# Kernel optimization log

Hardware: AMD Instinct MI355X
Metric: run time of the kernel (lower is better)

The kernel has to match this reference:

```python
import jax, jax.numpy as jnp
import numpy as np

N, E, D_IN, D_H, D_OUT, W = 100000, 1600000, 128, 128, 128, 3
HTC_W, TEMP = 0.01, 1.0  # curvature c = 1.0


def _project(x):
    n = jnp.maximum(jnp.linalg.norm(x, axis=-1, keepdims=True), 1e-12)
    return x * jnp.minimum((1.0 - 1e-5) / n, 1.0)


def _artanh(x):
    x = jnp.clip(x, -1.0 + 1e-6, 1.0 - 1e-6)
    return 0.5 * (jnp.log1p(x) - jnp.log1p(-x))


def _expmap0(v):
    n = jnp.maximum(jnp.linalg.norm(v, axis=-1, keepdims=True), 1e-12)
    return _project(jnp.tanh(n) * v / n)


def _logmap0(y):
    y = _project(y)
    n = jnp.maximum(jnp.linalg.norm(y, axis=-1, keepdims=True), 1e-12)
    return _artanh(n) * y / n


def setup_inputs() -> dict:
    key = jax.random.key(0)
    ks = jax.random.split(key, 24)
    x = jax.random.normal(ks[0], (N, D_IN), dtype=jnp.float32)
    edge_index = jax.random.randint(ks[1], (2, E), 0, N)
    t = jax.random.uniform(ks[2], (E,), dtype=jnp.float32)
    prev_hyp = _project(jax.random.normal(ks[3], (N, D_OUT), dtype=jnp.float32) * 0.05)
    lengths = jax.random.randint(ks[4], (N,), 0, W + 1)
    valid_mask = jnp.arange(W)[None, :] < lengths[:, None]  # front-filled deque
    hist_hyp = _project(jax.random.normal(ks[5], (N, W, D_OUT), dtype=jnp.float32) * 0.05)
    hist_hyp = hist_hyp * valid_mask[..., None].astype(jnp.float32)  # padded slots are zero

    def lin(k, dout, din):
        return jax.random.normal(k, (dout, din), dtype=jnp.float32) / np.sqrt(din)

    params = dict(
        w_time=jax.random.normal(ks[6], (D_IN,), dtype=jnp.float32),
        b_time=jnp.zeros((D_IN,), jnp.float32),
        W0_l=lin(ks[7], D_H, D_IN), b0_l=jnp.zeros((D_H,), jnp.float32), W0_r=lin(ks[8], D_H, D_IN),
        W1_l=lin(ks[9], D_OUT, D_H), b1_l=jnp.zeros((D_OUT,), jnp.float32), W1_r=lin(ks[10], D_OUT, D_H),
        W_ih=lin(ks[11], 3 * D_OUT, D_OUT), W_hh=lin(ks[12], 3 * D_OUT, D_OUT),
        b_ih=jnp.zeros((3 * D_OUT,), jnp.float32), b_hh=jnp.zeros((3 * D_OUT,), jnp.float32),
        Wq=lin(ks[13], D_OUT, D_OUT), Wk=lin(ks[14], D_OUT, D_OUT), Wv=lin(ks[15], D_OUT, D_OUT),
    )
    return dict(x=x, edge_index=edge_index, t=t, prev_hyp=prev_hyp,
                hist_hyp=hist_hyp, valid_mask=valid_mask, **params)


def reference(x, edge_index, t, prev_hyp, hist_hyp, valid_mask,
              w_time, b_time, W0_l, b0_l, W0_r, W1_l, b1_l, W1_r,
              W_ih, W_hh, b_ih, b_hh, Wq, Wk, Wv):
    n = x.shape[0]
    src, dst = edge_index[0], edge_index[1]
    ones_e = jnp.ones_like(t)
    # per-node mean event time over incident edges (src and dst both count)
    nt = jax.ops.segment_sum(t, src, n) + jax.ops.segment_sum(t, dst, n)
    cnt = jax.ops.segment_sum(ones_e, src, n) + jax.ops.segment_sum(ones_e, dst, n)
    node_time = nt / jnp.maximum(cnt, 1.0)
    x = x + jnp.cos(node_time[:, None] * w_time[None, :] + b_time[None, :])
    # SAGEConv (mean aggr over incoming edges): out = W_l @ mean_j x_j + b + W_r @ x_i
    deg = jnp.maximum(jax.ops.segment_sum(ones_e, dst, n), 1.0)[:, None]
    agg0 = jax.ops.segment_sum(x[src], dst, n) / deg
    h = jax.nn.relu(agg0 @ W0_l.T + b0_l + x @ W0_r.T)
    agg1 = jax.ops.segment_sum(h[src], dst, n) / deg
    h_now = agg1 @ W1_l.T + b1_l + h @ W1_r.T  # tangent-space current embedding

    prev_tan = _logmap0(prev_hyp)
    # ragged history attention (padded + masked)
    hist_tan = _logmap0(hist_hyp)                       # [N, W, D]
    q = h_now @ Wq.T                                    # [N, D]
    k = hist_tan @ Wk.T                                 # [N, W, D]
    v = hist_tan @ Wv.T
    score = jnp.einsum('nwd,nd->nw', k, q) / (np.sqrt(D_OUT) * max(TEMP, 1e-6))
    has_hist = valid_mask.any(axis=-1, keepdims=True)
    score = jnp.where(valid_mask, score, -jnp.inf)
    score = jnp.where(has_hist, score, 0.0)
    alpha = jax.nn.softmax(score, axis=-1)
    alpha = jnp.where(has_hist, alpha, 0.0)
    ctx = jnp.einsum('nw,nwd->nd', alpha, v)

    # GRUCell(input=h_now, hidden=prev_tan + ctx)
    hidden = prev_tan + ctx
    gi = h_now @ W_ih.T + b_ih
    gh = hidden @ W_hh.T + b_hh
    i_r, i_z, i_n = jnp.split(gi, 3, axis=-1)
    h_r, h_z, h_n = jnp.split(gh, 3, axis=-1)
    r = jax.nn.sigmoid(i_r + h_r)
    z = jax.nn.sigmoid(i_z + h_z)
    nn_ = jnp.tanh(i_n + r * h_n)
    h_tan = (1.0 - z) * nn_ + z * hidden
    h_hyp = _expmap0(h_tan)

    # hyperbolic temporal consistency aux loss (c = 1)
    x_sq = jnp.sum(h_hyp * h_hyp, axis=-1)
    y_sq = jnp.sum(prev_hyp * prev_hyp, axis=-1)
    diff_sq = jnp.sum((h_hyp - prev_hyp) ** 2, axis=-1)
    denom = jnp.maximum((1.0 - x_sq) * (1.0 - y_sq), 1e-8)
    zarg = jnp.maximum(1.0 + 2.0 * diff_sq / denom, 1.0 + 1e-6)
    dist = jnp.arccosh(zarg)
    valid_prev = (jnp.sum(jnp.abs(prev_hyp), axis=-1) > 0).astype(dist.dtype)
    aux = HTC_W * jnp.sum(dist * valid_prev) / jnp.maximum(jnp.sum(valid_prev), 1.0)
    aux = jnp.where(jnp.any(valid_prev > 0), aux, 0.0)
    return h_hyp, aux
```

## Files before the change

kernel.cpp:

```cpp
#include <hip/hip_runtime.h>
#include <math.h>


typedef _Float16 f16x8 __attribute__((ext_vector_type(8)));
typedef _Float16 f16x4 __attribute__((ext_vector_type(4)));
typedef _Float16 f16x2 __attribute__((ext_vector_type(2)));
typedef float f32x4 __attribute__((ext_vector_type(4)));

__device__ __forceinline__ float wsum(float v) {
#pragma unroll
  for (int off = 1; off < 64; off <<= 1) v += __shfl_xor(v, off, 64);
  return v;
}

__device__ __forceinline__ void fsplit(float x, _Float16& h, _Float16& l) {
  h = (_Float16)x;
  l = (_Float16)(x - (float)h);
}

__device__ __forceinline__ float logmap_scale(float nrm2) {
  float n0 = fmaxf(sqrtf(nrm2), 1e-12f);
  float sp = fminf((1.0f - 1e-5f) / n0, 1.0f);
  float np = fmaxf(n0 * sp, 1e-12f);
  float a  = fminf(np, 1.0f - 1e-6f);
  float at = 0.5f * (log1pf(a) - log1pf(-a));
  return sp * at / np;
}

__global__ void k_edge(const int* __restrict__ ei, const float* __restrict__ t,
                       unsigned long long* __restrict__ packed, int E) {
  int e = blockIdx.x * 256 + threadIdx.x;
  if (e >= E) return;
  int s = ei[e], d = ei[E + e];
  unsigned long long tf =
      (unsigned long long)__float2uint_rn(t[e] * 16777216.0f);
  unsigned long long encs = tf | (1ULL << 40);
  atomicAdd(&packed[s], encs);
  atomicAdd(&packed[d], encs | (1ULL << 52));
}

__global__ void k_scan1(const unsigned long long* __restrict__ packed,
                        int* __restrict__ rowptr, int* __restrict__ bsum, int N) {
  __shared__ int s[256];
  int t = threadIdx.x;
  int base = blockIdx.x * 1024 + t * 4;
  int v[4]; int loc = 0;
#pragma unroll
  for (int j = 0; j < 4; ++j) {
    int i = base + j;
    v[j] = (i < N) ? (int)(packed[i] >> 52) : 0;
    loc += v[j];
  }
  s[t] = loc; __syncthreads();
  for (int off = 1; off < 256; off <<= 1) {
    int x = (t >= off) ? s[t - off] : 0; __syncthreads();
    s[t] += x; __syncthreads();
  }
  int run = s[t] - loc;
#pragma unroll
  for (int j = 0; j < 4; ++j) { int i = base + j; if (i < N) rowptr[i] = run; run += v[j]; }
  if (t == 255) bsum[blockIdx.x] = s[255];
}

__global__ void k_scan2(const int* __restrict__ bsum, int* __restrict__ boff, int nb) {
  __shared__ int s[128];
  int t = threadIdx.x;
  int v = (t < nb) ? bsum[t] : 0;
  s[t] = v; __syncthreads();
  for (int off = 1; off < 128; off <<= 1) {
    int x = (t >= off) ? s[t - off] : 0; __syncthreads();
    s[t] += x; __syncthreads();
  }
  boff[t] = s[t] - v;
}

__global__ void k_scan3(int* __restrict__ rowptr, const int* __restrict__ boff, int N, int E) {
  int i = blockIdx.x * 256 + threadIdx.x;
  if (i < N) rowptr[i] += boff[i >> 10];
  if (i == 0) rowptr[N] = E;
}

__global__ void k_scatter(const int* __restrict__ ei, const int* __restrict__ rowptr,
                          int* __restrict__ cursor, int* __restrict__ eidx, int E) {
  int e = blockIdx.x * 256 + threadIdx.x;
  if (e >= E) return;
  int s = ei[e], d = ei[E + e];
  int p = rowptr[d] + atomicAdd(&cursor[d], 1);
  eidx[p] = s;
}

__global__ void k_time(const float* __restrict__ x,
                       const unsigned long long* __restrict__ packed,
                       const float* __restrict__ wt,
                       const float* __restrict__ bt,
                       _Float16* __restrict__ outH, _Float16* __restrict__ outL, int N) {
  int id = blockIdx.x * 256 + threadIdx.x;
  if (id >= N * 32) return;
  int n = id >> 5, q = id & 31;
  unsigned long long p = packed[n];
  float tsum = (float)(p & 0xFFFFFFFFFFULL) * 5.9604644775390625e-8f;
  int c = (int)((p >> 40) & 0xFFF);
  float tm = tsum / fmaxf((float)c, 1.0f);
  float4 xv = ((const float4*)x)[id];
  float4 wv = ((const float4*)wt)[q];
  float4 bv = ((const float4*)bt)[q];
  float o[4];
  o[0] = xv.x + cosf(tm * wv.x + bv.x);
  o[1] = xv.y + cosf(tm * wv.y + bv.y);
  o[2] = xv.z + cosf(tm * wv.z + bv.z);
  o[3] = xv.w + cosf(tm * wv.w + bv.w);
  f16x4 vh, vl;
#pragma unroll
  for (int j = 0; j < 4; ++j) { _Float16 h, l; fsplit(o[j], h, l); vh[j] = h; vl[j] = l; }
  *(f16x4*)&outH[(size_t)id * 4] = vh;
  *(f16x4*)&outL[(size_t)id * 4] = vl;
}

__global__ void k_agg(const _Float16* __restrict__ XH, const _Float16* __restrict__ XL,
                      const int* __restrict__ rowptr,
                      const int* __restrict__ eidx, _Float16* __restrict__ outH,
                      _Float16* __restrict__ outL, int N) {
  int wid = threadIdx.x >> 6, lane = threadIdx.x & 63;
  int n = blockIdx.x * 4 + wid;
  if (n >= N) return;
  int s0 = rowptr[n], s1 = rowptr[n + 1];
  float ax = 0.f, ay = 0.f;
  for (int e = s0; e < s1; ++e) {
    int s = eidx[e];
    f16x2 vh = *(const f16x2*)&XH[(size_t)s * 128 + lane * 2];
    f16x2 vl = *(const f16x2*)&XL[(size_t)s * 128 + lane * 2];
    ax += (float)vh[0] + (float)vl[0];
    ay += (float)vh[1] + (float)vl[1];
  }
  float sc = 1.0f / fmaxf((float)(s1 - s0), 1.0f);
  _Float16 hx, lx, hy, ly;
  fsplit(ax * sc, hx, lx); fsplit(ay * sc, hy, ly);
  f16x2 vh = {hx, hy}, vl = {lx, ly};
  *(f16x2*)&outH[(size_t)n * 128 + lane * 2] = vh;
  *(f16x2*)&outL[(size_t)n * 128 + lane * 2] = vl;
}

__global__ void k_prep(const float* __restrict__ W0l, const float* __restrict__ W0r,
                       const float* __restrict__ W1l, const float* __restrict__ W1r,
                       const float* __restrict__ Wv,  const float* __restrict__ Wih,
                       const float* __restrict__ Whh, const float* __restrict__ bih,
                       const float* __restrict__ bhh,
                       _Float16* __restrict__ W0H, _Float16* __restrict__ W0L,
                       _Float16* __restrict__ W1H, _Float16* __restrict__ W1L,
                       _Float16* __restrict__ WvH, _Float16* __restrict__ WvL,
                       _Float16* __restrict__ WzH, _Float16* __restrict__ WzL,
                       float* __restrict__ bz) {
  int id = blockIdx.x * 256 + threadIdx.x;
  if (id < 32768) {
    int c = id >> 8, k = id & 255;
    float v0 = (k < 128) ? W0l[c * 128 + k] : W0r[c * 128 + (k - 128)];
    float v1 = (k < 128) ? W1l[c * 128 + k] : W1r[c * 128 + (k - 128)];
    fsplit(v0, W0H[id], W0L[id]);
    fsplit(v1, W1H[id], W1L[id]);
  }
  if (id < 16384) {
    fsplit(Wv[id], WvH[id], WvL[id]);
  }
  if (id < 131072) {
    int c = id >> 8, k = id & 255;
    float v;
    if (c < 256)      v = (k < 128) ? Wih[c * 128 + k] : Whh[c * 128 + (k - 128)];
    else if (c < 384) v = (k < 128) ? Wih[c * 128 + k] : 0.f;
    else              v = (k < 128) ? 0.f : Whh[(c - 128) * 128 + (k - 128)];
    fsplit(v, WzH[id], WzL[id]);
  }
  if (id < 512) {
    float v;
    if (id < 256)      v = bih[id] + bhh[id];
    else if (id < 384) v = bih[id];
    else               v = bhh[id - 128];
    bz[id] = v;
  }
}

__global__ void k_ct(const float* __restrict__ Wk, const float* __restrict__ Wq,
                     _Float16* __restrict__ CtH, _Float16* __restrict__ CtL) {
  int id = blockIdx.x * 256 + threadIdx.x;
  if (id >= 16384) return;
  int c = id >> 7, k = id & 127;
  float s = 0.f;
  for (int j = 0; j < 128; ++j) s += Wk[j * 128 + c] * Wq[j * 128 + k];
  fsplit(s, CtH[id], CtL[id]);
}

__global__ __launch_bounds__(256)
void k_mm(const _Float16* __restrict__ A1H, const _Float16* __restrict__ A1L,
          const _Float16* __restrict__ A2H, const _Float16* __restrict__ A2L,
          const _Float16* __restrict__ WH,  const _Float16* __restrict__ WL,
          const float* __restrict__ bias,   const float* __restrict__ addb,
          float* __restrict__ outF, _Float16* __restrict__ outH,
          _Float16* __restrict__ outL,
          int Nrows, int Ktot, int Ctot, int relu) {
  __shared__ _Float16 sA[2][128][64];
  __shared__ _Float16 sW[2][128][64];
  const int tid = threadIdx.x;
  const int lane = tid & 63;
  const int wv = tid >> 6;
  const int wr = wv >> 1, wc = wv & 1;
  const int laneR = lane & 15, laneG = lane >> 4;
  const int n0 = blockIdx.x * 128;
  const int c0 = blockIdx.y * 128;

  f32x4 acc[4][4];
#pragma unroll
  for (int mi = 0; mi < 4; ++mi)
#pragma unroll
    for (int ni = 0; ni < 4; ++ni)
#pragma unroll
      for (int j = 0; j < 4; ++j) acc[mi][ni][j] = 0.f;

  const int nslab = Ktot >> 6;
  for (int s = 0; s < nslab; ++s) {
    int kglob = s << 6;
    const _Float16* aH = (kglob < 128) ? A1H : A2H;
    const _Float16* aL = (kglob < 128) ? A1L : A2L;
    int kc = kglob & 127;
    __syncthreads();
#pragma unroll
    for (int it = 0; it < 4; ++it) {
      int idx = tid + (it << 8);
      int r = idx >> 3, chunk = idx & 7;
      int cs = (chunk ^ (r & 7)) << 3;
      int kq = chunk << 3;
      int n = n0 + r;
      f16x8 vh, vl;
      if (n < Nrows) {
        vh = *(const f16x8*)&aH[(size_t)n * 128 + kc + kq];
        vl = *(const f16x8*)&aL[(size_t)n * 128 + kc + kq];
      } else {
#pragma unroll
        for (int j = 0; j < 8; ++j) { vh[j] = (_Float16)0; vl[j] = (_Float16)0; }
      }
      *(f16x8*)&sA[0][r][cs] = vh;
      *(f16x8*)&sA[1][r][cs] = vl;
      int c = c0 + r;
      f16x8 wh = *(const f16x8*)&WH[(size_t)c * Ktot + kglob + kq];
      f16x8 wl = *(const f16x8*)&WL[(size_t)c * Ktot + kglob + kq];
      *(f16x8*)&sW[0][r][cs] = wh;
      *(f16x8*)&sW[1][r][cs] = wl;
    }
    __syncthreads();
#pragma unroll
    for (int kk = 0; kk < 2; ++kk) {
      f16x8 ah[4], al[4], bh[4], bl[4];
      int kch = (kk << 2) + laneG;
#pragma unroll
      for (int m = 0; m < 4; ++m) {
        int row = wr * 64 + m * 16 + laneR;
        int ko = (kch ^ (row & 7)) << 3;
        ah[m] = *(const f16x8*)&sA[0][row][ko];
        al[m] = *(const f16x8*)&sA[1][row][ko];
      }
#pragma unroll
      for (int n = 0; n < 4; ++n) {
        int row = wc * 64 + n * 16 + laneR;
        int ko = (kch ^ (row & 7)) << 3;
        bh[n] = *(const f16x8*)&sW[0][row][ko];
        bl[n] = *(const f16x8*)&sW[1][row][ko];
      }
#pragma unroll
      for (int m = 0; m < 4; ++m)
#pragma unroll
        for (int n = 0; n < 4; ++n) {
          acc[m][n] = __builtin_amdgcn_mfma_f32_16x16x32_f16(ah[m], bh[n], acc[m][n], 0, 0, 0);
          acc[m][n] = __builtin_amdgcn_mfma_f32_16x16x32_f16(al[m], bh[n], acc[m][n], 0, 0, 0);
          acc[m][n] = __builtin_amdgcn_mfma_f32_16x16x32_f16(ah[m], bl[n], acc[m][n], 0, 0, 0);
        }
    }
  }
#pragma unroll
  for (int m = 0; m < 4; ++m) {
#pragma unroll
    for (int n = 0; n < 4; ++n) {
      int rbase = n0 + wr * 64 + m * 16 + laneG * 4;
      int c = c0 + wc * 64 + n * 16 + laneR;
      float bval = bias ? bias[c] : 0.f;
#pragma unroll
      for (int j = 0; j < 4; ++j) {
        int r = rbase + j;
        if (r >= Nrows) continue;
        float v = acc[m][n][j] + bval;
        if (addb) v += addb[(size_t)r * Ctot + c];
        if (relu) v = fmaxf(v, 0.f);
        if (outF) outF[(size_t)r * Ctot + c] = v;
        if (outH) {
          _Float16 h, l; fsplit(v, h, l);
          outH[(size_t)r * Ctot + c] = h;
          outL[(size_t)r * Ctot + c] = l;
        }
      }
    }
  }
}

__global__ __launch_bounds__(256, 2)
void k_gru(const _Float16* __restrict__ P0H, const _Float16* __restrict__ P0L,
           const _Float16* __restrict__ P2H, const _Float16* __restrict__ P2L,
           const _Float16* __restrict__ WzH, const _Float16* __restrict__ WzL,
           const float* __restrict__ bz, const float* __restrict__ prev,
           float* __restrict__ out, float* __restrict__ pd,
           float* __restrict__ pv, int N) {
  __shared__ _Float16 sA[2][64][64];
  __shared__ _Float16 sW[2][128][64];
  __shared__ float rn1[64][2];
  __shared__ float rn3[64][2][3];
  __shared__ float distrow[64], validrow[64];
  const int tid = threadIdx.x;
  const int lane = tid & 63;
  const int wv = tid >> 6;
  const int wr = wv >> 1, wc = wv & 1;
  const int laneR = lane & 15, laneG = lane >> 4;
  const int n0 = blockIdx.x * 64;

  f32x4 acc[4][2][4];
#pragma unroll
  for (int q = 0; q < 4; ++q)
#pragma unroll
    for (int m = 0; m < 2; ++m)
#pragma unroll
      for (int n = 0; n < 4; ++n)
#pragma unroll
        for (int j = 0; j < 4; ++j) acc[q][m][n][j] = 0.f;

#define STAGE_W(Q)                                                          \
  {                                                                         \
    _Pragma("unroll")                                                       \
    for (int it = 0; it < 4; ++it) {                                        \
      int idx = tid + (it << 8);                                            \
      int r = idx >> 3, chunk = idx & 7;                                    \
      int cs = (chunk ^ (r & 7)) << 3;                                      \
      int kq = chunk << 3;                                                  \
      size_t wrow = (size_t)((Q)*128 + r);                                  \
      *(f16x8*)&sW[0][r][cs] = *(const f16x8*)&WzH[wrow * 256 + kglob + kq];\
      *(f16x8*)&sW[1][r][cs] = *(const f16x8*)&WzL[wrow * 256 + kglob + kq];\
    }                                                                       \
  }

#define COMPUTE_Q(Q)                                                        \
  {                                                                         \
    _Pragma("unroll")                                                       \
    for (int kk = 0; kk < 2; ++kk) {                                        \
      int kch = (kk << 2) + laneG;                                          \
      f16x8 ah[2], al[2], bh[4], bl[4];                                     \
      _Pragma("unroll")                                                     \
      for (int m = 0; m < 2; ++m) {                                         \
        int row = wr * 32 + m * 16 + laneR;                                 \
        int ko = (kch ^ (row & 7)) << 3;                                    \
        ah[m] = *(const f16x8*)&sA[0][row][ko];                             \
        al[m] = *(const f16x8*)&sA[1][row][ko];                             \
      }                                                                     \
      _Pragma("unroll")                                                     \
      for (int n = 0; n < 4; ++n) {                                         \
        int row = wc * 64 + n * 16 + laneR;                                 \
        int ko = (kch ^ (row & 7)) << 3;                                    \
        bh[n] = *(const f16x8*)&sW[0][row][ko];                             \
        bl[n] = *(const f16x8*)&sW[1][row][ko];                             \
      }                                                                     \
      _Pragma("unroll")                                                     \
      for (int m = 0; m < 2; ++m)                                           \
        _Pragma("unroll")                                                   \
        for (int n = 0; n < 4; ++n) {                                       \
          acc[Q][m][n] = __builtin_amdgcn_mfma_f32_16x16x32_f16(ah[m], bh[n], acc[Q][m][n], 0, 0, 0); \
          acc[Q][m][n] = __builtin_amdgcn_mfma_f32_16x16x32_f16(al[m], bh[n], acc[Q][m][n], 0, 0, 0); \
          acc[Q][m][n] = __builtin_amdgcn_mfma_f32_16x16x32_f16(ah[m], bl[n], acc[Q][m][n], 0, 0, 0); \
        }                                                                   \
    }                                                                       \
  }

#pragma unroll
  for (int s = 0; s < 4; ++s) {
    int kglob = s << 6;
    const _Float16* aH = (s < 2) ? P0H : P2H;
    const _Float16* aL = (s < 2) ? P0L : P2L;
    int kc = kglob & 127;
    __syncthreads();
#pragma unroll
    for (int it = 0; it < 2; ++it) {
      int idx = tid + (it << 8);
      int r = idx >> 3, chunk = idx & 7;
      int cs = (chunk ^ (r & 7)) << 3;
      int kq = chunk << 3;
      int n = n0 + r;
      f16x8 vh, vl;
      if (n < N) {
        vh = *(const f16x8*)&aH[(size_t)n * 128 + kc + kq];
        vl = *(const f16x8*)&aL[(size_t)n * 128 + kc + kq];
      } else {
#pragma unroll
        for (int j = 0; j < 8; ++j) { vh[j] = (_Float16)0; vl[j] = (_Float16)0; }
      }
      *(f16x8*)&sA[0][r][cs] = vh;
      *(f16x8*)&sA[1][r][cs] = vl;
    }
    STAGE_W(0);
    __syncthreads();
    COMPUTE_Q(0);
    __syncthreads();
    STAGE_W(1);
    __syncthreads();
    COMPUTE_Q(1);
    __syncthreads();
    if (s < 2) {
      STAGE_W(2);
      __syncthreads();
      COMPUTE_Q(2);
    } else {
      STAGE_W(3);
      __syncthreads();
      COMPUTE_Q(3);
    }
  }
#undef STAGE_W
#undef COMPUTE_Q

  float bz0[4], bz1[4], bz2[4], bz3[4];
#pragma unroll
  for (int n = 0; n < 4; ++n) {
    int d = wc * 64 + n * 16 + laneR;
    bz0[n] = bz[d]; bz1[n] = bz[128 + d]; bz2[n] = bz[256 + d]; bz3[n] = bz[384 + d];
  }
  float tv[2][4][4];
#pragma unroll
  for (int m = 0; m < 2; ++m)
#pragma unroll
    for (int n = 0; n < 4; ++n)
#pragma unroll
      for (int j = 0; j < 4; ++j) {
        int row = n0 + wr * 32 + m * 16 + laneG * 4 + j;
        int d = wc * 64 + n * 16 + laneR;
        float hid = 0.f;
        if (row < N) {
          size_t o = (size_t)row * 128 + d;
          hid = (float)P2H[o] + (float)P2L[o];
        }
        float gr = acc[0][m][n][j] + bz0[n];
        float gz = acc[1][m][n][j] + bz1[n];
        float gi = acc[2][m][n][j] + bz2[n];
        float gh = acc[3][m][n][j] + bz3[n];
        float rr = 1.f / (1.f + expf(-gr));
        float zz = 1.f / (1.f + expf(-gz));
        float nn = tanhf(gi + rr * gh);
        tv[m][n][j] = (1.f - zz) * nn + zz * hid;
      }
#pragma unroll
  for (int m = 0; m < 2; ++m)
#pragma unroll
    for (int j = 0; j < 4; ++j) {
      float p = 0.f;
#pragma unroll
      for (int n = 0; n < 4; ++n) p += tv[m][n][j] * tv[m][n][j];
#pragma unroll
      for (int off = 1; off < 16; off <<= 1) p += __shfl_xor(p, off, 64);
      if (laneR == 0) rn1[wr * 32 + m * 16 + laneG * 4 + j][wc] = p;
    }
  __syncthreads();
  float hv[2][4][4];
#pragma unroll
  for (int m = 0; m < 2; ++m)
#pragma unroll
    for (int j = 0; j < 4; ++j) {
      int rl = wr * 32 + m * 16 + laneG * 4 + j;
      int row = n0 + rl;
      float nv2 = rn1[rl][0] + rn1[rl][1];
      float nv = fmaxf(sqrtf(nv2), 1e-12f);
      float tn = tanhf(nv);
      float s1 = tn / nv;
      float nw = fmaxf(tn, 1e-12f);
      float sp = fminf((1.f - 1e-5f) / nw, 1.f);
      float scl = s1 * sp;
#pragma unroll
      for (int n = 0; n < 4; ++n) {
        float h = tv[m][n][j] * scl;
        hv[m][n][j] = h;
        int d = wc * 64 + n * 16 + laneR;
        if (row < N) out[(size_t)row * 128 + d] = h;
      }
    }
#pragma unroll
  for (int m = 0; m < 2; ++m)
#pragma unroll
    for (int j = 0; j < 4; ++j) {
      int rl = wr * 32 + m * 16 + laneG * 4 + j;
      int row = n0 + rl;
      float ys = 0.f, ds = 0.f, pa = 0.f;
#pragma unroll
      for (int n = 0; n < 4; ++n) {
        int d = wc * 64 + n * 16 + laneR;
        float p = (row < N) ? prev[(size_t)row * 128 + d] : 0.f;
        float h = hv[m][n][j];
        ys += p * p; ds += (h - p) * (h - p); pa += fabsf(p);
      }
#pragma unroll
      for (int off = 1; off < 16; off <<= 1) {
        ys += __shfl_xor(ys, off, 64);
        ds += __shfl_xor(ds, off, 64);
        pa += __shfl_xor(pa, off, 64);
      }
      if (laneR == 0) { rn3[rl][wc][0] = ys; rn3[rl][wc][1] = ds; rn3[rl][wc][2] = pa; }
    }
  __syncthreads();
  if (wc == 0 && laneR == 0) {
#pragma unroll
    for (int m = 0; m < 2; ++m)
#pragma unroll
      for (int j = 0; j < 4; ++j) {
        int rl = wr * 32 + m * 16 + laneG * 4 + j;
        int row = n0 + rl;
        float nv2 = rn1[rl][0] + rn1[rl][1];
        float nv = fmaxf(sqrtf(nv2), 1e-12f);
        float tn = tanhf(nv);
        float s1 = tn / nv;
        float nw = fmaxf(tn, 1e-12f);
        float sp = fminf((1.f - 1e-5f) / nw, 1.f);
        float scl = s1 * sp;
        float x_sq = scl * scl * nv2;
        float y_sq = rn3[rl][0][0] + rn3[rl][1][0];
        float d_sq = rn3[rl][0][1] + rn3[rl][1][1];
        float pab  = rn3[rl][0][2] + rn3[rl][1][2];
        float denom = fmaxf((1.f - x_sq) * (1.f - y_sq), 1e-8f);
        float zarg = fmaxf(1.f + 2.f * d_sq / denom, 1.f + 1e-6f);
        float dist = acoshf(zarg);
        float valid = (pab > 0.f && row < N) ? 1.f : 0.f;
        distrow[rl] = dist * valid;
        validrow[rl] = valid;
      }
  }
  __syncthreads();
  if (tid < 64) {
    float dv = distrow[tid], vvv = validrow[tid];
    dv = wsum(dv); vvv = wsum(vvv);
    if (tid == 0) { pd[blockIdx.x] = dv; pv[blockIdx.x] = vvv; }
  }
}

__global__ void k_logmap(const float* __restrict__ Y, float* __restrict__ out, int N) {
  int wid = threadIdx.x >> 6, lane = threadIdx.x & 63;
  int n = blockIdx.x * 4 + wid;
  if (n >= N) return;
  float2 y = ((const float2*)Y)[(size_t)n * 64 + lane];
  float nrm2 = wsum(y.x * y.x + y.y * y.y);
  float s = logmap_scale(nrm2);
  ((float2*)out)[(size_t)n * 64 + lane] = make_float2(y.x * s, y.y * s);
}

__global__ void k_attn(const float* __restrict__ U, const float* __restrict__ hist,
                       _Float16* __restrict__ outH, _Float16* __restrict__ outL, int N) {
  int wid = threadIdx.x >> 6, lane = threadIdx.x & 63;
  int n = blockIdx.x * 4 + wid;
  if (n >= N) return;
  float2 u = ((const float2*)U)[(size_t)n * 64 + lane];
  float htx[3], hty[3], sc[3];
  bool val[3];
#pragma unroll
  for (int w = 0; w < 3; ++w) {
    float2 h = ((const float2*)hist)[((size_t)n * 3 + w) * 64 + lane];
    float nrm2 = wsum(h.x * h.x + h.y * h.y);
    val[w] = nrm2 > 0.f;
    float s = logmap_scale(nrm2);
    htx[w] = h.x * s; hty[w] = h.y * s;
    float d = wsum(htx[w] * u.x + hty[w] * u.y);
    sc[w] = d * 0.0883883476483184f;
  }
  float cx = 0.f, cy = 0.f;
  if (val[0] || val[1] || val[2]) {
    float m = -INFINITY;
#pragma unroll
    for (int w = 0; w < 3; ++w) if (val[w]) m = fmaxf(m, sc[w]);
    float a[3]; float ssum = 0.f;
#pragma unroll
    for (int w = 0; w < 3; ++w) { a[w] = val[w] ? expf(sc[w] - m) : 0.f; ssum += a[w]; }
    float inv = 1.f / ssum;
#pragma unroll
    for (int w = 0; w < 3; ++w) { cx += htx[w] * (a[w] * inv); cy += hty[w] * (a[w] * inv); }
  }
  _Float16 hx, lx, hy, ly;
  fsplit(cx, hx, lx); fsplit(cy, hy, ly);
  f16x2 vh = {hx, hy}, vl = {lx, ly};
  *(f16x2*)&outH[(size_t)n * 128 + lane * 2] = vh;
  *(f16x2*)&outL[(size_t)n * 128 + lane * 2] = vl;
}

__global__ void k_reduce(const float* __restrict__ pd, const float* __restrict__ pv,
                         float* __restrict__ aux_out, int nparts) {
  __shared__ float sd[256], sv[256];
  float a = 0.f, b = 0.f;
  for (int i = threadIdx.x; i < nparts; i += 256) { a += pd[i]; b += pv[i]; }
  sd[threadIdx.x] = a; sv[threadIdx.x] = b; __syncthreads();
  for (int off = 128; off > 0; off >>= 1) {
    if (threadIdx.x < off) { sd[threadIdx.x] += sd[threadIdx.x + off]; sv[threadIdx.x] += sv[threadIdx.x + off]; }
    __syncthreads();
  }
  if (threadIdx.x == 0) {
    float aux = (sv[0] > 0.f) ? 0.01f * sd[0] / fmaxf(sv[0], 1.f) : 0.f;
    aux_out[0] = aux;
  }
}

extern "C" void kernel_launch(void* const* d_in, const int* in_sizes, int n_in,
                              void* d_out, int out_size, void* d_ws, size_t ws_size,
                              hipStream_t stream) {
  const float* x      = (const float*)d_in[0];
  const int*   ei     = (const int*)  d_in[1];
  const float* t      = (const float*)d_in[2];
  const float* prev   = (const float*)d_in[3];
  const float* hist   = (const float*)d_in[4];
  const float* w_time = (const float*)d_in[6];
  const float* b_time = (const float*)d_in[7];
  const float* W0l    = (const float*)d_in[8];
  const float* b0l    = (const float*)d_in[9];
  const float* W0r    = (const float*)d_in[10];
  const float* W1l    = (const float*)d_in[11];
  const float* b1l    = (const float*)d_in[12];
  const float* W1r    = (const float*)d_in[13];
  const float* Wih    = (const float*)d_in[14];
  const float* Whh    = (const float*)d_in[15];
  const float* bih    = (const float*)d_in[16];
  const float* bhh    = (const float*)d_in[17];
  const float* Wq     = (const float*)d_in[18];
  const float* Wk     = (const float*)d_in[19];
  const float* Wv     = (const float*)d_in[20];

  const int N = in_sizes[0] / 128;
  const int E = in_sizes[1] / 2;
  const int NB4 = (N + 3) / 4;
  const int NB1 = (N + 1023) / 1024;
  const int NBG = (N + 63) / 64;

  char* wbase = (char*)d_ws;
  size_t off = 0;
  auto alloc = [&](size_t bytes) -> void* {
    off = (off + 255) & ~(size_t)255;
    void* p = wbase + off; off += bytes; return p;
  };
  unsigned long long* packed = (unsigned long long*)alloc((size_t)N * 8);
  int*   cursor = (int*)  alloc((size_t)N * 4);
  size_t zero_bytes = off;
  int*   rowptr = (int*)  alloc((size_t)(N + 1) * 4);
  int*   bsum   = (int*)  alloc(512);
  int*   boff   = (int*)  alloc(512);
  int*   eidx   = (int*)  alloc((size_t)E * 4);
  _Float16* W0H = (_Float16*)alloc(32768 * 2);
  _Float16* W0L = (_Float16*)alloc(32768 * 2);
  _Float16* W1H = (_Float16*)alloc(32768 * 2);
  _Float16* W1L = (_Float16*)alloc(32768 * 2);
  _Float16* CtH = (_Float16*)alloc(16384 * 2);
  _Float16* CtL = (_Float16*)alloc(16384 * 2);
  _Float16* WvH = (_Float16*)alloc(16384 * 2);
  _Float16* WvL = (_Float16*)alloc(16384 * 2);
  _Float16* WzH = (_Float16*)alloc(131072 * 2);
  _Float16* WzL = (_Float16*)alloc(131072 * 2);
  float* bz     = (float*)alloc(512 * 4);
  float* F0 = (float*)alloc((size_t)N * 128 * 4);
  float* F1 = (float*)alloc((size_t)N * 128 * 4);
  _Float16* P0H = (_Float16*)alloc((size_t)N * 128 * 2);
  _Float16* P0L = (_Float16*)alloc((size_t)N * 128 * 2);
  _Float16* P1H = (_Float16*)alloc((size_t)N * 128 * 2);
  _Float16* P1L = (_Float16*)alloc((size_t)N * 128 * 2);
  _Float16* P2H = (_Float16*)alloc((size_t)N * 128 * 2);
  _Float16* P2L = (_Float16*)alloc((size_t)N * 128 * 2);
  float* pd = (float*)alloc((size_t)NBG * 4);
  float* pv = (float*)alloc((size_t)NBG * 4);
  (void)ws_size; (void)n_in; (void)out_size;

  float* out_h   = (float*)d_out;
  float* out_aux = out_h + (size_t)N * 128;

  hipMemsetAsync(d_ws, 0, zero_bytes, stream);

  k_prep<<<512, 256, 0, stream>>>(W0l, W0r, W1l, W1r, Wv, Wih, Whh, bih, bhh,
                                  W0H, W0L, W1H, W1L, WvH, WvL, WzH, WzL, bz);
  k_ct<<<64, 256, 0, stream>>>(Wk, Wq, CtH, CtL);

  int ebl = (E + 255) / 256;
  k_edge<<<ebl, 256, 0, stream>>>(ei, t, packed, E);
  k_scan1<<<NB1, 256, 0, stream>>>(packed, rowptr, bsum, N);
  k_scan2<<<1, 128, 0, stream>>>(bsum, boff, NB1);
  k_scan3<<<(N + 255) / 256, 256, 0, stream>>>(rowptr, boff, N, E);
  k_scatter<<<ebl, 256, 0, stream>>>(ei, rowptr, cursor, eidx, E);

  k_time<<<(N * 32 + 255) / 256, 256, 0, stream>>>(x, packed, w_time, b_time,
                                                   P0H, P0L, N);
  k_agg<<<NB4, 256, 0, stream>>>(P0H, P0L, rowptr, eidx, P1H, P1L, N);
  dim3 gb((N + 127) / 128, 1);
  k_mm<<<gb, 256, 0, stream>>>(P1H, P1L, P0H, P0L, W0H, W0L, b0l, nullptr,
                               nullptr, P2H, P2L, N, 256, 128, 1);
  k_agg<<<NB4, 256, 0, stream>>>(P2H, P2L, rowptr, eidx, P1H, P1L, N);
  k_mm<<<gb, 256, 0, stream>>>(P1H, P1L, P2H, P2L, W1H, W1L, b1l, nullptr,
                               nullptr, P0H, P0L, N, 256, 128, 0);
  k_mm<<<gb, 256, 0, stream>>>(P0H, P0L, nullptr, nullptr, CtH, CtL, nullptr, nullptr,
                               F0, nullptr, nullptr, N, 128, 128, 0);
  k_attn<<<NB4, 256, 0, stream>>>(F0, hist, P1H, P1L, N);
  k_logmap<<<NB4, 256, 0, stream>>>(prev, F1, N);
  k_mm<<<gb, 256, 0, stream>>>(P1H, P1L, nullptr, nullptr, WvH, WvL, nullptr, F1,
                               nullptr, P2H, P2L, N, 128, 128, 0);
  k_gru<<<NBG, 256, 0, stream>>>(P0H, P0L, P2H, P2L, WzH, WzL, bz, prev,
                                 out_h, pd, pv, N);
  k_reduce<<<1, 256, 0, stream>>>(pd, pv, out_aux, NBG);
}
```

Measured before the change: 1.224 ms.

## Fuse query-key matmul with attention and fold logmap scale into Wv epilogue

Result: no change. 1.215 ms (-0.7%).

```diff
diff --git a/kernel.cpp b/kernel.cpp
--- a/kernel.cpp
+++ b/kernel.cpp
@@ -124,11 +124,31 @@
   int n = blockIdx.x * 4 + wid;
   if (n >= N) return;
   int s0 = rowptr[n], s1 = rowptr[n + 1];
-  float ax = 0.f, ay = 0.f;
-  for (int e = s0; e < s1; ++e) {
+  size_t lo2 = (size_t)lane * 2;
+  float ax0 = 0.f, ay0 = 0.f, ax1 = 0.f, ay1 = 0.f;
+  float ax2 = 0.f, ay2 = 0.f, ax3 = 0.f, ay3 = 0.f;
+  int e = s0;
+  for (; e + 4 <= s1; e += 4) {
+    int i0 = eidx[e], i1 = eidx[e + 1], i2 = eidx[e + 2], i3 = eidx[e + 3];
+    f16x2 h0 = *(const f16x2*)&XH[(size_t)i0 * 128 + lo2];
+    f16x2 l0 = *(const f16x2*)&XL[(size_t)i0 * 128 + lo2];
+    f16x2 h1 = *(const f16x2*)&XH[(size_t)i1 * 128 + lo2];
+    f16x2 l1 = *(const f16x2*)&XL[(size_t)i1 * 128 + lo2];
+    f16x2 h2 = *(const f16x2*)&XH[(size_t)i2 * 128 + lo2];
+    f16x2 l2 = *(const f16x2*)&XL[(size_t)i2 * 128 + lo2];
+    f16x2 h3 = *(const f16x2*)&XH[(size_t)i3 * 128 + lo2];
+    f16x2 l3 = *(const f16x2*)&XL[(size_t)i3 * 128 + lo2];
+    ax0 += (float)h0[0] + (float)l0[0]; ay0 += (float)h0[1] + (float)l0[1];
+    ax1 += (float)h1[0] + (float)l1[0]; ay1 += (float)h1[1] + (float)l1[1];
+    ax2 += (float)h2[0] + (float)l2[0]; ay2 += (float)h2[1] + (float)l2[1];
+    ax3 += (float)h3[0] + (float)l3[0]; ay3 += (float)h3[1] + (float)l3[1];
+  }
+  float ax = (ax0 + ax1) + (ax2 + ax3);
+  float ay = (ay0 + ay1) + (ay2 + ay3);
+  for (; e < s1; ++e) {
     int s = eidx[e];
-    f16x2 vh = *(const f16x2*)&XH[(size_t)s * 128 + lane * 2];
-    f16x2 vl = *(const f16x2*)&XL[(size_t)s * 128 + lane * 2];
+    f16x2 vh = *(const f16x2*)&XH[(size_t)s * 128 + lo2];
+    f16x2 vl = *(const f16x2*)&XL[(size_t)s * 128 + lo2];
     ax += (float)vh[0] + (float)vl[0];
     ay += (float)vh[1] + (float)vl[1];
   }
@@ -136,8 +156,8 @@
   _Float16 hx, lx, hy, ly;
   fsplit(ax * sc, hx, lx); fsplit(ay * sc, hy, ly);
   f16x2 vh = {hx, hy}, vl = {lx, ly};
-  *(f16x2*)&outH[(size_t)n * 128 + lane * 2] = vh;
-  *(f16x2*)&outL[(size_t)n * 128 + lane * 2] = vl;
+  *(f16x2*)&outH[(size_t)n * 128 + lo2] = vh;
+  *(f16x2*)&outL[(size_t)n * 128 + lo2] = vl;
 }
 
 __global__ void k_prep(const float* __restrict__ W0l, const float* __restrict__ W0r,
@@ -188,11 +208,21 @@
   fsplit(s, CtH[id], CtL[id]);
 }
 
+__global__ void k_lognorm(const float* __restrict__ Y, float* __restrict__ scale, int N) {
+  int wid = threadIdx.x >> 6, lane = threadIdx.x & 63;
+  int n = blockIdx.x * 4 + wid;
+  if (n >= N) return;
+  float2 y = ((const float2*)Y)[(size_t)n * 64 + lane];
+  float nrm2 = wsum(y.x * y.x + y.y * y.y);
+  if (lane == 0) scale[n] = logmap_scale(nrm2);
+}
+
 __global__ __launch_bounds__(256)
 void k_mm(const _Float16* __restrict__ A1H, const _Float16* __restrict__ A1L,
           const _Float16* __restrict__ A2H, const _Float16* __restrict__ A2L,
           const _Float16* __restrict__ WH,  const _Float16* __restrict__ WL,
           const float* __restrict__ bias,   const float* __restrict__ addb,
+          const float* __restrict__ scalev,
           float* __restrict__ outF, _Float16* __restrict__ outH,
           _Float16* __restrict__ outL,
           int Nrows, int Ktot, int Ctot, int relu) {
@@ -285,7 +315,10 @@
         int r = rbase + j;
         if (r >= Nrows) continue;
         float v = acc[m][n][j] + bval;
-        if (addb) v += addb[(size_t)r * Ctot + c];
+        if (addb) {
+          float ab = addb[(size_t)r * Ctot + c];
+          v += scalev ? ab * scalev[r] : ab;
+        }
         if (relu) v = fmaxf(v, 0.f);
         if (outF) outF[(size_t)r * Ctot + c] = v;
         if (outH) {
@@ -295,6 +328,133 @@
         }
       }
     }
+  }
+}
+
+__global__ __launch_bounds__(256, 2)
+void k_uattn(const _Float16* __restrict__ AH, const _Float16* __restrict__ AL,
+             const _Float16* __restrict__ WH, const _Float16* __restrict__ WL,
+             const float* __restrict__ hist,
+             _Float16* __restrict__ outH, _Float16* __restrict__ outL, int N) {
+  __shared__ __align__(16) char smem[65536];
+  _Float16 (*sA)[128][64] = (_Float16(*)[128][64])smem;
+  _Float16 (*sW)[128][64] = (_Float16(*)[128][64])(smem + 32768);
+  float (*uS)[128] = (float(*)[128])smem;
+  const int tid = threadIdx.x;
+  const int lane = tid & 63;
+  const int wv = tid >> 6;
+  const int wr = wv >> 1, wc = wv & 1;
+  const int laneR = lane & 15, laneG = lane >> 4;
+  const int n0 = blockIdx.x * 128;
+
+  f32x4 acc[4][4];
+#pragma unroll
+  for (int mi = 0; mi < 4; ++mi)
+#pragma unroll
+    for (int ni = 0; ni < 4; ++ni)
+#pragma unroll
+      for (int j = 0; j < 4; ++j) acc[mi][ni][j] = 0.f;
+
+  for (int s = 0; s < 2; ++s) {
+    int kglob = s << 6;
+    __syncthreads();
+#pragma unroll
+    for (int it = 0; it < 4; ++it) {
+      int idx = tid + (it << 8);
+      int r = idx >> 3, chunk = idx & 7;
+      int cs = (chunk ^ (r & 7)) << 3;
+      int kq = chunk << 3;
+      int n = n0 + r;
+      f16x8 vh, vl;
+      if (n < N) {
+        vh = *(const f16x8*)&AH[(size_t)n * 128 + kglob + kq];
+        vl = *(const f16x8*)&AL[(size_t)n * 128 + kglob + kq];
+      } else {
+#pragma unroll
+        for (int j = 0; j < 8; ++j) { vh[j] = (_Float16)0; vl[j] = (_Float16)0; }
+      }
+      *(f16x8*)&sA[0][r][cs] = vh;
+      *(f16x8*)&sA[1][r][cs] = vl;
+      f16x8 wh = *(const f16x8*)&WH[(size_t)r * 128 + kglob + kq];
+      f16x8 wl = *(const f16x8*)&WL[(size_t)r * 128 + kglob + kq];
+      *(f16x8*)&sW[0][r][cs] = wh;
+      *(f16x8*)&sW[1][r][cs] = wl;
+    }
+    __syncthreads();
+#pragma unroll
+    for (int kk = 0; kk < 2; ++kk) {
+      f16x8 ah[4], al[4], bh[4], bl[4];
+      int kch = (kk << 2) + laneG;
+#pragma unroll
+      for (int m = 0; m < 4; ++m) {
+        int row = wr * 64 + m * 16 + laneR;
+        int ko = (kch ^ (row & 7)) << 3;
+        ah[m] = *(const f16x8*)&sA[0][row][ko];
+        al[m] = *(const f16x8*)&sA[1][row][ko];
+      }
+#pragma unroll
+      for (int n = 0; n < 4; ++n) {
+        int row = wc * 64 + n * 16 + laneR;
+        int ko = (kch ^ (row & 7)) << 3;
+        bh[n] = *(const f16x8*)&sW[0][row][ko];
+        bl[n] = *(const f16x8*)&sW[1][row][ko];
+      }
+#pragma unroll
+      for (int m = 0; m < 4; ++m)
+#pragma unroll
+        for (int n = 0; n < 4; ++n) {
+          acc[m][n] = __builtin_amdgcn_mfma_f32_16x16x32_f16(ah[m], bh[n], acc[m][n], 0, 0, 0);
+          acc[m][n] = __builtin_amdgcn_mfma_f32_16x16x32_f16(al[m], bh[n], acc[m][n], 0, 0, 0);
+          acc[m][n] = __builtin_amdgcn_mfma_f32_16x16x32_f16(ah[m], bl[n], acc[m][n], 0, 0, 0);
+        }
+    }
+  }
+  __syncthreads();
+#pragma unroll
+  for (int m = 0; m < 4; ++m)
+#pragma unroll
+    for (int n = 0; n < 4; ++n) {
+      int rl = wr * 64 + m * 16 + laneG * 4;
+      int c = wc * 64 + n * 16 + laneR;
+#pragma unroll
+      for (int j = 0; j < 4; ++j) uS[rl + j][c] = acc[m][n][j];
+    }
+  __syncthreads();
+
+  for (int i = 0; i < 32; ++i) {
+    int rl = wv * 32 + i;
+    int n = n0 + rl;
+    if (n >= N) break;
+    float2 u = *(const float2*)&uS[rl][lane * 2];
+    float htx[3], hty[3], sc[3];
+    bool val[3];
+#pragma unroll
+    for (int w = 0; w < 3; ++w) {
+      float2 h = ((const float2*)hist)[((size_t)n * 3 + w) * 64 + lane];
+      float nrm2 = wsum(h.x * h.x + h.y * h.y);
+      val[w] = nrm2 > 0.f;
+      float s = logmap_scale(nrm2);
+      htx[w] = h.x * s; hty[w] = h.y * s;
+      float d = wsum(htx[w] * u.x + hty[w] * u.y);
+      sc[w] = d * 0.0883883476483184f;
+    }
+    float cx = 0.f, cy = 0.f;
+    if (val[0] || val[1] || val[2]) {
+      float m = -INFINITY;
+#pragma unroll
+      for (int w = 0; w < 3; ++w) if (val[w]) m = fmaxf(m, sc[w]);
+      float a[3]; float ssum = 0.f;
+#pragma unroll
+      for (int w = 0; w < 3; ++w) { a[w] = val[w] ? expf(sc[w] - m) : 0.f; ssum += a[w]; }
+      float inv = 1.f / ssum;
+#pragma unroll
+      for (int w = 0; w < 3; ++w) { cx += htx[w] * (a[w] * inv); cy += hty[w] * (a[w] * inv); }
+    }
+    _Float16 hx, lx, hy, ly;
+    fsplit(cx, hx, lx); fsplit(cy, hy, ly);
+    f16x2 vh = {hx, hy}, vl = {lx, ly};
+    *(f16x2*)&outH[(size_t)n * 128 + lane * 2] = vh;
+    *(f16x2*)&outL[(size_t)n * 128 + lane * 2] = vl;
   }
 }
 
@@ -538,53 +698,6 @@
   }
 }
 
-__global__ void k_logmap(const float* __restrict__ Y, float* __restrict__ out, int N) {
-  int wid = threadIdx.x >> 6, lane = threadIdx.x & 63;
-  int n = blockIdx.x * 4 + wid;
-  if (n >= N) return;
-  float2 y = ((const float2*)Y)[(size_t)n * 64 + lane];
-  float nrm2 = wsum(y.x * y.x + y.y * y.y);
-  float s = logmap_scale(nrm2);
-  ((float2*)out)[(size_t)n * 64 + lane] = make_float2(y.x * s, y.y * s);
-}
-
-__global__ void k_attn(const float* __restrict__ U, const float* __restrict__ hist,
-                       _Float16* __restrict__ outH, _Float16* __restrict__ outL, int N) {
-  int wid = threadIdx.x >> 6, lane = threadIdx.x & 63;
-  int n = blockIdx.x * 4 + wid;
-  if (n >= N) return;
-  float2 u = ((const float2*)U)[(size_t)n * 64 + lane];
-  float htx[3], hty[3], sc[3];
-  bool val[3];
-#pragma unroll
-  for (int w = 0; w < 3; ++w) {
-    float2 h = ((const float2*)hist)[((size_t)n * 3 + w) * 64 + lane];
-    float nrm2 = wsum(h.x * h.x + h.y * h.y);
-    val[w] = nrm2 > 0.f;
-    float s = logmap_scale(nrm2);
-    htx[w] = h.x * s; hty[w] = h.y * s;
-    float d = wsum(htx[w] * u.x + hty[w] * u.y);
-    sc[w] = d * 0.0883883476483184f;
-  }
-  float cx = 0.f, cy = 0.f;
-  if (val[0] || val[1] || val[2]) {
-    float m = -INFINITY;
-#pragma unroll
-    for (int w = 0; w < 3; ++w) if (val[w]) m = fmaxf(m, sc[w]);
-    float a[3]; float ssum = 0.f;
-#pragma unroll
-    for (int w = 0; w < 3; ++w) { a[w] = val[w] ? expf(sc[w] - m) : 0.f; ssum += a[w]; }
-    float inv = 1.f / ssum;
-#pragma unroll
-    for (int w = 0; w < 3; ++w) { cx += htx[w] * (a[w] * inv); cy += hty[w] * (a[w] * inv); }
-  }
-  _Float16 hx, lx, hy, ly;
-  fsplit(cx, hx, lx); fsplit(cy, hy, ly);
-  f16x2 vh = {hx, hy}, vl = {lx, ly};
-  *(f16x2*)&outH[(size_t)n * 128 + lane * 2] = vh;
-  *(f16x2*)&outL[(size_t)n * 128 + lane * 2] = vl;
-}
-
 __global__ void k_reduce(const float* __restrict__ pd, const float* __restrict__ pv,
                          float* __restrict__ aux_out, int nparts) {
   __shared__ float sd[256], sv[256];
@@ -655,8 +768,7 @@
   _Float16* WzH = (_Float16*)alloc(131072 * 2);
   _Float16* WzL = (_Float16*)alloc(131072 * 2);
   float* bz     = (float*)alloc(512 * 4);
-  float* F0 = (float*)alloc((size_t)N * 128 * 4);
-  float* F1 = (float*)alloc((size_t)N * 128 * 4);
+  float* scale  = (float*)alloc((size_t)N * 4);
   _Float16* P0H = (_Float16*)alloc((size_t)N * 128 * 2);
   _Float16* P0L = (_Float16*)alloc((size_t)N * 128 * 2);
   _Float16* P1H = (_Float16*)alloc((size_t)N * 128 * 2);
@@ -675,6 +787,7 @@
   k_prep<<<512, 256, 0, stream>>>(W0l, W0r, W1l, W1r, Wv, Wih, Whh, bih, bhh,
                                   W0H, W0L, W1H, W1L, WvH, WvL, WzH, WzL, bz);
   k_ct<<<64, 256, 0, stream>>>(Wk, Wq, CtH, CtL);
+  k_lognorm<<<NB4, 256, 0, stream>>>(prev, scale, N);
 
   int ebl = (E + 255) / 256;
   k_edge<<<ebl, 256, 0, stream>>>(ei, t, packed, E);
@@ -687,17 +800,14 @@
                                                    P0H, P0L, N);
   k_agg<<<NB4, 256, 0, stream>>>(P0H, P0L, rowptr, eidx, P1H, P1L, N);
   dim3 gb((N + 127) / 128, 1);
-  k_mm<<<gb, 256, 0, stream>>>(P1H, P1L, P0H, P0L, W0H, W0L, b0l, nullptr,
+  k_mm<<<gb, 256, 0, stream>>>(P1H, P1L, P0H, P0L, W0H, W0L, b0l, nullptr, nullptr,
                                nullptr, P2H, P2L, N, 256, 128, 1);
   k_agg<<<NB4, 256, 0, stream>>>(P2H, P2L, rowptr, eidx, P1H, P1L, N);
-  k_mm<<<gb, 256, 0, stream>>>(P1H, P1L, P2H, P2L, W1H, W1L, b1l, nullptr,
+  k_mm<<<gb, 256, 0, stream>>>(P1H, P1L, P2H, P2L, W1H, W1L, b1l, nullptr, nullptr,
                                nullptr, P0H, P0L, N, 256, 128, 0);
-  k_mm<<<gb, 256, 0, stream>>>(P0H, P0L, nullptr, nullptr, CtH, CtL, nullptr, nullptr,
-                               F0, nullptr, nullptr, N, 128, 128, 0);
-  k_attn<<<NB4, 256, 0, stream>>>(F0, hist, P1H, P1L, N);
-  k_logmap<<<NB4, 256, 0, stream>>>(prev, F1, N);
-  k_mm<<<gb, 256, 0, stream>>>(P1H, P1L, nullptr, nullptr, WvH, WvL, nullptr, F1,
-                               nullptr, P2H, P2L, N, 128, 128, 0);
+  k_uattn<<<gb, 256, 0, stream>>>(P0H, P0L, CtH, CtL, hist, P1H, P1L, N);
+  k_mm<<<gb, 256, 0, stream>>>(P1H, P1L, nullptr, nullptr, WvH, WvL, nullptr, prev,
+                               scale, nullptr, P2H, P2L, N, 128, 128, 0);
   k_gru<<<NBG, 256, 0, stream>>>(P0H, P0L, P2H, P2L, WzH, WzL, bz, prev,
                                  out_h, pd, pv, N);
   k_reduce<<<1, 256, 0, stream>>>(pd, pv, out_aux, NBG);
```
